# Optimization experiments

Hardware: AMD Instinct MI355X
Metric: run time of the kernel (lower is better)

The kernel has to match this reference:

```python
import jax, jax.numpy as jnp
import numpy as np

K = 3
KK = K * K
EPS = 1e-5


def conv2d(x, w, b, pad):
    y = jax.lax.conv_general_dilated(x, w, (1, 1), [(pad, pad), (pad, pad)],
                                     dimension_numbers=("NCHW", "OIHW", "NCHW"))
    return y + b[None, :, None, None]


def bn(x, g, b, m, v):
    inv = g / jnp.sqrt(v + EPS)
    return x * inv[None, :, None, None] + (b - m * inv)[None, :, None, None]


def deform_sample(x, dy, dx):
    # x: [B,C,H,W]; dy,dx: [B,KK,H,W] -> sampled [B,C,KK,H,W] (bilinear, zeros outside)
    B, C, H, W = x.shape
    k = jnp.arange(K, dtype=x.dtype) - 1.0  # pad=1, dilation=1, stride=1
    ky = jnp.repeat(k, K)  # [KK] row offsets
    kx = jnp.tile(k, K)    # [KK] col offsets
    hh = jnp.arange(H, dtype=x.dtype)
    ww = jnp.arange(W, dtype=x.dtype)
    py = hh[None, :, None] + ky[:, None, None] + dy  # [B,KK,H,W]
    px = ww[None, None, :] + kx[:, None, None] + dx

    def sample_one(img, py, px):
        y0f = jnp.floor(py); x0f = jnp.floor(px)
        wy = py - y0f; wx = px - x0f
        y0 = y0f.astype(jnp.int32); x0 = x0f.astype(jnp.int32)

        def gather(yi, xi, w):
            valid = (yi >= 0) & (yi < H) & (xi >= 0) & (xi < W)
            yc = jnp.clip(yi, 0, H - 1); xc = jnp.clip(xi, 0, W - 1)
            v = img[:, yc, xc]  # [C,KK,H,W]
            return v * (w * valid)[None]

        return (gather(y0, x0, (1 - wy) * (1 - wx)) +
                gather(y0, x0 + 1, (1 - wy) * wx) +
                gather(y0 + 1, x0, wy * (1 - wx)) +
                gather(y0 + 1, x0 + 1, wy * wx))

    return jax.vmap(sample_one)(x, py, px)


def setup_inputs() -> dict:
    key = jax.random.key(0)
    ks = jax.random.split(key, 16)
    B, C, H, W = 8, 256, 64, 64
    d = {
        "feature": jax.random.normal(ks[0], (B, C, H, W), jnp.float32),
        "p1_w": jax.random.normal(ks[1], (C, C, 1, 1), jnp.float32) * 0.05,
        "p1_b": jax.random.normal(ks[2], (C,), jnp.float32) * 0.05,
        "bn1_g": jax.random.normal(ks[3], (C,), jnp.float32) * 0.1 + 1.0,
        "bn1_b": jax.random.normal(ks[4], (C,), jnp.float32) * 0.05,
        "bn1_m": jax.random.normal(ks[5], (C,), jnp.float32) * 0.05,
        "bn1_v": jax.random.uniform(ks[6], (C,), jnp.float32) + 0.5,
        "off_w": jax.random.normal(ks[7], (3 * KK, 2 * C, K, K), jnp.float32) * 0.01,
        "off_b": jax.random.normal(ks[8], (3 * KK,), jnp.float32) * 0.01,
        "dcn_w": jax.random.normal(ks[9], (C, C, K, K), jnp.float32) * 0.05,
        "dcn_b": jax.random.normal(ks[10], (C,), jnp.float32) * 0.05,
        "bn2_g": jax.random.normal(ks[11], (C,), jnp.float32) * 0.1 + 1.0,
        "bn2_b": jax.random.normal(ks[12], (C,), jnp.float32) * 0.05,
        "bn2_m": jax.random.normal(ks[13], (C,), jnp.float32) * 0.05,
        "bn2_v": jax.random.uniform(ks[14], (C,), jnp.float32) + 0.5,
    }
    return d


def reference(feature, p1_w, p1_b, bn1_g, bn1_b, bn1_m, bn1_v,
              off_w, off_b, dcn_w, dcn_b, bn2_g, bn2_b, bn2_m, bn2_v):
    flipped = feature[..., ::-1]                      # flip last (W) axis
    proj = bn(conv2d(feature, p1_w, p1_b, 0), bn1_g, bn1_b, bn1_m, bn1_v)
    # DCNv2: offsets/mask from concat(flipped, proj)
    concat = jnp.concatenate([flipped, proj], axis=1)
    off = conv2d(concat, off_w, off_b, 1)             # [B,27,H,W]
    dy = off[:, :KK]
    dx = off[:, KK:2 * KK]
    mask = jax.nn.sigmoid(off[:, 2 * KK:])            # [B,KK,H,W]
    sampled = deform_sample(flipped, dy, dx)          # [B,C,KK,H,W]
    O = dcn_w.shape[0]
    y = jnp.einsum("bckhw,ock->bohw", sampled * mask[:, None], dcn_w.reshape(O, -1, KK))
    y = y + dcn_b[None, :, None, None]
    y = bn(y, bn2_g, bn2_b, bn2_m, bn2_v)
    return jax.nn.relu(proj + y)
```

## Files before the change

### kernel.cpp

```cpp
#include <hip/hip_runtime.h>
#include <hip/hip_bf16.h>
#include <math.h>

typedef __attribute__((ext_vector_type(8))) short short8;
typedef __attribute__((ext_vector_type(4))) short short4v;
typedef __attribute__((ext_vector_type(4))) float f32x4;
typedef __attribute__((ext_vector_type(2))) float f32x2;

__device__ __forceinline__ float bs2f(short s){
    union { unsigned u; float f; } x; x.u = ((unsigned)(unsigned short)s) << 16; return x.f;
}
__device__ __forceinline__ short f2bs(float f){
    union { float f; unsigned u; } x; x.f = f;
    unsigned r = x.u + 0x7fff + ((x.u >> 16) & 1);
    return (short)(r >> 16);
}
__device__ __forceinline__ f32x2 up2(unsigned u){
    union { unsigned u; float f; } lo, hi;
    lo.u = u << 16; hi.u = u & 0xffff0000u;
    f32x2 r; r.x = lo.f; r.y = hi.f; return r;
}
__device__ __forceinline__ unsigned pk2rn(float lo, float hi){
    __hip_bfloat162 h = __float22bfloat162_rn(make_float2(lo, hi));
    union { __hip_bfloat162 h; unsigned u; } cv; cv.h = h; return cv.u;
}
__device__ __forceinline__ void gl2lds16(const void* g, void* l){
    __builtin_amdgcn_global_load_lds(
        (const __attribute__((address_space(1))) void*)g,
        (__attribute__((address_space(3))) void*)l, 16, 0, 0);
}
__device__ __forceinline__ void hard_barrier(){
    __builtin_amdgcn_sched_barrier(0);
    __builtin_amdgcn_s_barrier();
    __builtin_amdgcn_sched_barrier(0);
}

#define XPB ((size_t)66*66*512)


__global__ void k_prep(const float* __restrict__ p1_w, const float* __restrict__ p1_b,
                       const float* __restrict__ bn1_g, const float* __restrict__ bn1_b,
                       const float* __restrict__ bn1_m, const float* __restrict__ bn1_v,
                       const float* __restrict__ off_w,
                       const float* __restrict__ dcn_w, const float* __restrict__ dcn_b,
                       const float* __restrict__ bn2_g, const float* __restrict__ bn2_b,
                       const float* __restrict__ bn2_m, const float* __restrict__ bn2_v,
                       short* __restrict__ p1_wb, short* __restrict__ Woffb,
                       short* __restrict__ Wbf,
                       float* __restrict__ bias1f, float* __restrict__ inv2f,
                       float* __restrict__ bias2f, unsigned* __restrict__ XpadU)
{
    int blk = blockIdx.x, t = threadIdx.x;
    if (blk == 0) {
        float inv1 = bn1_g[t] / sqrtf(bn1_v[t] + 1e-5f);
        bias1f[t] = p1_b[t] * inv1 + bn1_b[t] - bn1_m[t] * inv1;
        float inv2 = bn2_g[t] / sqrtf(bn2_v[t] + 1e-5f);
        inv2f[t] = inv2;
        bias2f[t] = dcn_b[t] * inv2 + bn2_b[t] - bn2_m[t] * inv2;
    } else if (blk <= 256) {
        int ci = blk - 1;
        float inv1 = bn1_g[t] / sqrtf(bn1_v[t] + 1e-5f);
        p1_wb[t*256 + ci] = f2bs(p1_w[t*256 + ci] * inv1);
    } else if (blk <= 2560) {
        int ck = blk - 257;
        int c = ck / 9, tap = ck % 9;
        Wbf[t*2304 + tap*256 + c] = f2bs(dcn_w[t*2304 + ck]);
    } else if (blk <= 7168) {
        int e = blk - 2561;
        if (t < 32) {
            int tap = e >> 9, ci = e & 511;
            float v = off_w[((t < 27) ? t : 0)*4608 + ci*9 + tap];
            Woffb[t*4608 + e] = (t < 27) ? f2bs(v) : (short)0;
        }
    } else {
        int hb = blk - 7169;
        int b = hb / 260, i = hb % 260;
        int y, x;
        if (i < 66)       { y = 0;  x = i; }
        else if (i < 132) { y = 65; x = i - 66; }
        else { int j = i - 132; y = 1 + (j >> 1); x = (j & 1) * 65; }
        XpadU[((size_t)(b*66 + y)*66 + x)*256 + t] = 0u;
    }
}

__global__ void k_featT(const float* __restrict__ feature, short* __restrict__ Xpad)
{
    __shared__ float tile[64][65];
    int bb = blockIdx.x;
    int cg = bb & 3, h = (bb >> 2) & 63, b = bb >> 8;
    int c0 = cg * 64;
    int t = threadIdx.x;
    int lw = t & 63, li = t >> 6;
    #pragma unroll
    for (int j = 0; j < 16; ++j) {
        int cl = j*4 + li;
        tile[cl][63 - lw] = feature[((b*256 + c0 + cl)*64 + h)*64 + lw];
    }
    __syncthreads();
    #pragma unroll
    for (int j = 0; j < 16; ++j) {
        int wl = j*4 + li;
        Xpad[((size_t)(b*66 + h+1)*66 + (wl+1))*512 + c0 + lw] = f2bs(tile[lw][wl]);
    }
}

__global__ __launch_bounds__(512, 4) void k_projm(
    short* Xpad, const short* __restrict__ p1_wb, const float* __restrict__ bias1f)
{
    __shared__ short Ash[256*32];
    __shared__ short Bsh[64*32];
    int bid = blockIdx.x;
    int b = bid >> 6, h = bid & 63;
    int t = threadIdx.x;
    int lane = t & 63, w = t >> 6;
    int ln = lane & 15, q = lane >> 4;
    int r16 = lane >> 2;
    int sq  = (lane & 3) ^ ((lane >> 3) & 3);
    int rq  = (q ^ ((ln >> 1) & 3)) * 8;
    size_t rowbase = (size_t)(b*66 + h + 1)*66;

    f32x4 acc[2][4] = {};
    for (int kt = 0; kt < 8; ++kt) {
        int kcol = kt*32 + sq*8;
        #pragma unroll
        for (int i = 0; i < 2; ++i) {
            int row = w*32 + i*16 + r16;
            gl2lds16(p1_wb + (size_t)row*256 + kcol, Ash + (w*32 + i*16)*32);
        }
        if (w < 4) {
            int x = w*16 + r16;
            gl2lds16(Xpad + (rowbase + (64 - x))*512 + kcol, Bsh + (w*16)*32);
        }
        __syncthreads();
        short8 af[2], bfr[4];
        #pragma unroll
        for (int i = 0; i < 2; ++i)
            af[i] = *(const short8*)&Ash[(w*32 + i*16 + ln)*32 + rq];
        #pragma unroll
        for (int j = 0; j < 4; ++j)
            bfr[j] = *(const short8*)&Bsh[(j*16 + ln)*32 + rq];
        #pragma unroll
        for (int i = 0; i < 2; ++i)
            #pragma unroll
            for (int j = 0; j < 4; ++j)
                acc[i][j] = __builtin_amdgcn_mfma_f32_16x16x32_bf16(af[i], bfr[j], acc[i][j], 0, 0, 0);
        __syncthreads();
    }
    #pragma unroll
    for (int i = 0; i < 2; ++i) {
        int ob = w*32 + i*16 + q*4;
        #pragma unroll
        for (int j = 0; j < 4; ++j) {
            int x = j*16 + ln;
            size_t xb = (rowbase + x + 1)*512 + 256 + ob;
            short4v st;
            st.x = f2bs(acc[i][j][0] + bias1f[ob]);
            st.y = f2bs(acc[i][j][1] + bias1f[ob+1]);
            st.z = f2bs(acc[i][j][2] + bias1f[ob+2]);
            st.w = f2bs(acc[i][j][3] + bias1f[ob+3]);
            *(short4v*)&Xpad[xb] = st;
        }
    }
}

__global__ __launch_bounds__(512, 4) void k_offm(
    const short* __restrict__ Xpad, const short* __restrict__ Woffb,
    const float* __restrict__ off_b, float* __restrict__ offv)
{
    __shared__ short Ash[2][4][32*32];
    __shared__ short Bsh[2][4][64*32];
    int bid = blockIdx.x;
    int b = bid >> 6, h = bid & 63;
    int t = threadIdx.x;
    int lane = t & 63, w = t >> 6;
    int ln = lane & 15, q = lane >> 4;
    int wr = w >> 2, wc = w & 3;
    int r16 = lane >> 2;
    int sq  = (lane & 3) ^ ((lane >> 3) & 3);
    int rq  = (q ^ ((ln >> 1) & 3)) * 8;
    const short* xb = Xpad + (size_t)b*XPB;

    auto STAGE = [&](int it, int pb){
        int tap = it >> 2, c0 = (it & 3) << 7;
        int dy = tap/3 - 1, dx = tap%3 - 1;
        #pragma unroll
        for (int s = 0; s < 4; ++s) {
            int cc = c0 + s*32 + sq*8;
            if (w < 4) {
                int row = w*16 + r16;
                const short* gB = xb + ((size_t)(h + 1 + dy)*66 + (row + dx + 1))*512 + cc;
                gl2lds16(gB, &Bsh[pb][s][(w*16)*32]);
            } else if (w < 6) {
                int row = (w-4)*16 + r16;
                const short* gA = Woffb + (size_t)row*4608 + tap*512 + cc;
                gl2lds16(gA, &Ash[pb][s][((w-4)*16)*32]);
            }
        }
    };

    f32x4 acc = {};
    STAGE(0, 0);
    asm volatile("s_waitcnt vmcnt(0)" ::: "memory");
    hard_barrier();
    for (int it = 0; it < 36; ++it) {
        int pb = it & 1;
        if (it < 35) STAGE(it + 1, pb ^ 1);
        __builtin_amdgcn_sched_barrier(0);
        #pragma unroll
        for (int s = 0; s < 4; ++s) {
            short8 af  = *(const short8*)&Ash[pb][s][(wr*16 + ln)*32 + rq];
            short8 bfr = *(const short8*)&Bsh[pb][s][(wc*16 + ln)*32 + rq];
            acc = __builtin_amdgcn_mfma_f32_16x16x32_bf16(af, bfr, acc, 0, 0, 0);
        }
        asm volatile("s_waitcnt vmcnt(0) lgkmcnt(0)" ::: "memory");
        hard_barrier();
    }
    int x = wc*16 + ln;
    #pragma unroll
    for (int r = 0; r < 4; ++r) {
        int oc = wr*16 + q*4 + r;
        if (oc < 27)
            offv[((b*27 + oc)*64 + h)*64 + x] = acc[r] + off_b[oc];
    }
}

__global__ __launch_bounds__(512, 4) void k_gemm(
    const short* __restrict__ Xpad,
    const short* __restrict__ Wbf,
    const float* __restrict__ offv,
    const float* __restrict__ inv2f, const float* __restrict__ bias2f,
    float* __restrict__ out)
{
    __shared__ __align__(16) short Ash[2][256*32];
    __shared__ __align__(16) short Bsh[2][64*32];
    __shared__ unsigned c_pk[576];
    __shared__ float c_w[576*4];
    int bid = blockIdx.x;
    int b = bid & 7, h = bid >> 3;
    int t = threadIdx.x;
    int lane = t & 63, w = t >> 6;
    int ln = lane & 15, q = lane >> 4;
    int r16 = lane >> 2;
    int sq  = (lane & 3) ^ ((lane >> 3) & 3);
    int rq  = (q ^ ((ln >> 1) & 3)) * 8;

    for (int e = t; e < 576; e += 512) {
        int p = e / 9, k = e % 9;
        int base = (b*27)*4096 + h*64 + p;
        float dy = offv[base + k*4096];
        float dx = offv[base + (9+k)*4096];
        float ms = offv[base + (18+k)*4096];
        ms = 1.f / (1.f + expf(-ms));
        float py = (float)h + (float)(k/3 - 1) + dy;
        float px = (float)p + (float)(k%3 - 1) + dx;
        float y0f = floorf(py), x0f = floorf(px);
        float wy = py - y0f, wx = px - x0f;
        int y0 = (int)y0f, x0 = (int)x0f;
        int y1 = y0 + 1, x1 = x0 + 1;
        float vy0 = (y0 >= 0 && y0 < 64) ? 1.f : 0.f;
        float vy1 = (y1 >= 0 && y1 < 64) ? 1.f : 0.f;
        float vx0 = (x0 >= 0 && x0 < 64) ? 1.f : 0.f;
        float vx1 = (x1 >= 0 && x1 < 64) ? 1.f : 0.f;
        int y0c = min(max(y0,0),63), y1c = min(max(y1,0),63);
        int x0c = min(max(x0,0),63), x1c = min(max(x1,0),63);
        unsigned cell = (unsigned)(((y0c+1)*66 + x0c+1)*128);
        unsigned sx = (x1c != x0c) ? 1u : 0u;
        unsigned sy = (y1c != y0c) ? 1u : 0u;
        c_pk[e] = cell | (sx << 20) | (sy << 21);
        c_w[e*4+0] = ms * (1.f-wy)*(1.f-wx) * vy0*vx0;
        c_w[e*4+1] = ms * (1.f-wy)*wx       * vy0*vx1;
        c_w[e*4+2] = ms * wy*(1.f-wx)       * vy1*vx0;
        c_w[e*4+3] = ms * wy*wx             * vy1*vx1;
    }
    __syncthreads();

    const uint2* fT = (const uint2*)Xpad + (size_t)b*(XPB/4);
    int pr = t >> 3;
    int jo = t & 7;
    int pe9 = pr*9;
    short* bdst = &Bsh[jo >> 2][pr*32 + (((jo & 3) ^ ((pr >> 1) & 3)) << 3)];

    f32x4 acc[2][4] = {};
    uint4 U[4], V[4];

    auto GATHER = [&](int win, uint4 (&dst)[4]) {
        unsigned pw = c_pk[pe9 + (win >> 2)];
        int o00 = pw & 0xFFFFF;
        int dxs = (pw >> 13) & 128;
        int dys = ((pw >> 8) & 0x2000) | ((pw >> 13) & 0x100);
        int cin = ((win & 3) << 4) + jo*2;
        const uint2* p0 = fT + (o00 + cin);
        dst[0] = *(const uint4*)(p0);
        dst[1] = *(const uint4*)(p0 + dxs);
        dst[2] = *(const uint4*)(p0 + dys);
        dst[3] = *(const uint4*)(p0 + dys + dxs);
    };

    auto WIN = [&](int kc2, uint4 (&uc)[4], uint4 (&vn)[4]) {
        int tap = kc2 >> 2;
        #pragma unroll
        for (int s = 0; s < 2; ++s) {
            int kcol = (kc2*2 + s)*32 + sq*8;
            #pragma unroll
            for (int i = 0; i < 2; ++i) {
                int row = w*32 + i*16 + r16;
                gl2lds16(Wbf + (size_t)row*2304 + kcol, &Ash[s][(w*32 + i*16)*32]);
            }
        }
        __builtin_amdgcn_sched_barrier(0);
        GATHER(kc2 < 35 ? kc2 + 1 : 35, vn);
        const float4 cw = *(const float4*)&c_w[(pe9 + tap)*4];
        f32x2 Wx; Wx.x = cw.x; Wx.y = cw.x;
        f32x2 Wy; Wy.x = cw.y; Wy.y = cw.y;
        f32x2 Wz; Wz.x = cw.z; Wz.y = cw.z;
        f32x2 Ww; Ww.x = cw.w; Ww.y = cw.w;
        f32x2 G0 = Wx*up2(uc[0].x) + Wy*up2(uc[1].x) + Wz*up2(uc[2].x) + Ww*up2(uc[3].x);
        f32x2 G1 = Wx*up2(uc[0].y) + Wy*up2(uc[1].y) + Wz*up2(uc[2].y) + Ww*up2(uc[3].y);
        f32x2 G2 = Wx*up2(uc[0].z) + Wy*up2(uc[1].z) + Wz*up2(uc[2].z) + Ww*up2(uc[3].z);
        f32x2 G3 = Wx*up2(uc[0].w) + Wy*up2(uc[1].w) + Wz*up2(uc[2].w) + Ww*up2(uc[3].w);
        uint4 pkv;
        pkv.x = pk2rn(G0.x, G0.y);
        pkv.y = pk2rn(G1.x, G1.y);
        pkv.z = pk2rn(G2.x, G2.y);
        pkv.w = pk2rn(G3.x, G3.y);
        *(uint4*)bdst = pkv;
        asm volatile("s_waitcnt vmcnt(4) lgkmcnt(0)" ::: "memory");
        hard_barrier();
        #pragma unroll
        for (int s = 0; s < 2; ++s) {
            short8 af[2], bfr[4];
            #pragma unroll
            for (int i = 0; i < 2; ++i)
                af[i] = *(const short8*)&Ash[s][(w*32 + i*16 + ln)*32 + rq];
            #pragma unroll
            for (int jj = 0; jj < 4; ++jj)
                bfr[jj] = *(const short8*)&Bsh[s][(jj*16 + ln)*32 + rq];
            #pragma unroll
            for (int i = 0; i < 2; ++i)
                #pragma unroll
                for (int jj = 0; jj < 4; ++jj)
                    acc[i][jj] = __builtin_amdgcn_mfma_f32_16x16x32_bf16(af[i], bfr[jj], acc[i][jj], 0, 0, 0);
        }
        hard_barrier();
    };

    GATHER(0, U);
    __builtin_amdgcn_sched_barrier(0);
    for (int kc2 = 0; kc2 < 36; kc2 += 2) {
        WIN(kc2, U, V);
        WIN(kc2 + 1, V, U);
    }

    #pragma unroll
    for (int i = 0; i < 2; ++i) {
        int ob = w*32 + i*16 + q*4;
        #pragma unroll
        for (int jj = 0; jj < 4; ++jj) {
            int p = jj*16 + ln;
            size_t xb = ((size_t)(b*66 + h + 1)*66 + p + 1)*512 + 256 + ob;
            short4v prr = *(const short4v*)&Xpad[xb];
            #pragma unroll
            for (int r = 0; r < 4; ++r) {
                int o = ob + r;
                size_t idx = ((size_t)(b*256 + o))*4096 + h*64 + p;
                float rs = bs2f(((const short*)&prr)[r]);
                float v = rs + acc[i][jj][r]*inv2f[o] + bias2f[o];
                out[idx] = v < 0.f ? 0.f : v;
            }
        }
    }
}

extern "C" void kernel_launch(void* const* d_in, const int* in_sizes, int n_in,
                              void* d_out, int out_size, void* d_ws, size_t ws_size,
                              hipStream_t stream)
{
    const float* feature = (const float*)d_in[0];
    const float* p1_w  = (const float*)d_in[1];
    const float* p1_b  = (const float*)d_in[2];
    const float* bn1_g = (const float*)d_in[3];
    const float* bn1_b = (const float*)d_in[4];
    const float* bn1_m = (const float*)d_in[5];
    const float* bn1_v = (const float*)d_in[6];
    const float* off_w = (const float*)d_in[7];
    const float* off_b = (const float*)d_in[8];
    const float* dcn_w = (const float*)d_in[9];
    const float* dcn_b = (const float*)d_in[10];
    const float* bn2_g = (const float*)d_in[11];
    const float* bn2_b = (const float*)d_in[12];
    const float* bn2_m = (const float*)d_in[13];
    const float* bn2_v = (const float*)d_in[14];

    float* ws = (float*)d_ws;
    short* Xpad   = (short*)ws;
    float* offbuf = ws + 8921088;
    short* p1_wb  = (short*)(ws + 9805824);
    short* Woffb  = (short*)(ws + 9838592);
    short* Wbf    = (short*)(ws + 9912320);
    float* bias1f = ws + 10207232;
    float* inv2f  = ws + 10207488;
    float* bias2f = ws + 10207744;

    k_prep<<<9249, 256, 0, stream>>>(p1_w, p1_b, bn1_g, bn1_b, bn1_m, bn1_v,
                                     off_w, dcn_w, dcn_b, bn2_g, bn2_b, bn2_m, bn2_v,
                                     p1_wb, Woffb, Wbf, bias1f, inv2f, bias2f,
                                     (unsigned*)Xpad);
    k_featT<<<2048, 256, 0, stream>>>(feature, Xpad);
    k_projm<<<512, 512, 0, stream>>>(Xpad, p1_wb, bias1f);
    k_offm<<<512, 512, 0, stream>>>(Xpad, Woffb, off_b, offbuf);
    k_gemm<<<512, 512, 0, stream>>>(Xpad, Wbf, offbuf, inv2f, bias2f, (float*)d_out);
}
```

Measured before the change: 235.5 us.

## Load deform GEMM weights directly to registers and double-buffer sampled tiles

In k_gemm, the weight tile is no longer staged through LDS. Each wave loads its A fragments straight from global memory into registers one step ahead. The blended bilinear samples now go into a double-buffered LDS B tile, with the gather issued two steps ahead, so each window needs only one barrier. The offset-conv kernel drops its double buffering for a simpler single-buffer loop with two __syncthreads per iteration, and k_gemm's occupancy hint drops from 4 to 3 blocks for the extra registers. This trades register pressure and less latency hiding in k_offm for fewer barriers and less LDS traffic in the main GEMM.

```diff
diff --git a/kernel.cpp b/kernel.cpp
--- a/kernel.cpp
+++ b/kernel.cpp
@@ -31,6 +31,12 @@
 }
 __device__ __forceinline__ void hard_barrier(){
     __builtin_amdgcn_sched_barrier(0);
+    __builtin_amdgcn_s_barrier();
+    __builtin_amdgcn_sched_barrier(0);
+}
+__device__ __forceinline__ void lds_barrier(){
+    __builtin_amdgcn_sched_barrier(0);
+    asm volatile("s_waitcnt lgkmcnt(0)" ::: "memory");
     __builtin_amdgcn_s_barrier();
     __builtin_amdgcn_sched_barrier(0);
 }
@@ -167,8 +173,8 @@
     const short* __restrict__ Xpad, const short* __restrict__ Woffb,
     const float* __restrict__ off_b, float* __restrict__ offv)
 {
-    __shared__ short Ash[2][4][32*32];
-    __shared__ short Bsh[2][4][64*32];
+    __shared__ short Ash[4][32*32];
+    __shared__ short Bsh[4][64*32];
     int bid = blockIdx.x;
     int b = bid >> 6, h = bid & 63;
     int t = threadIdx.x;
@@ -180,7 +186,8 @@
     int rq  = (q ^ ((ln >> 1) & 3)) * 8;
     const short* xb = Xpad + (size_t)b*XPB;
 
-    auto STAGE = [&](int it, int pb){
+    f32x4 acc = {};
+    for (int it = 0; it < 36; ++it) {
         int tap = it >> 2, c0 = (it & 3) << 7;
         int dy = tap/3 - 1, dx = tap%3 - 1;
         #pragma unroll
@@ -189,31 +196,21 @@
             if (w < 4) {
                 int row = w*16 + r16;
                 const short* gB = xb + ((size_t)(h + 1 + dy)*66 + (row + dx + 1))*512 + cc;
-                gl2lds16(gB, &Bsh[pb][s][(w*16)*32]);
+                gl2lds16(gB, &Bsh[s][(w*16)*32]);
             } else if (w < 6) {
                 int row = (w-4)*16 + r16;
                 const short* gA = Woffb + (size_t)row*4608 + tap*512 + cc;
-                gl2lds16(gA, &Ash[pb][s][((w-4)*16)*32]);
+                gl2lds16(gA, &Ash[s][((w-4)*16)*32]);
             }
         }
-    };
-
-    f32x4 acc = {};
-    STAGE(0, 0);
-    asm volatile("s_waitcnt vmcnt(0)" ::: "memory");
-    hard_barrier();
-    for (int it = 0; it < 36; ++it) {
-        int pb = it & 1;
-        if (it < 35) STAGE(it + 1, pb ^ 1);
-        __builtin_amdgcn_sched_barrier(0);
+        __syncthreads();
         #pragma unroll
         for (int s = 0; s < 4; ++s) {
-            short8 af  = *(const short8*)&Ash[pb][s][(wr*16 + ln)*32 + rq];
-            short8 bfr = *(const short8*)&Bsh[pb][s][(wc*16 + ln)*32 + rq];
+            short8 af  = *(const short8*)&Ash[s][(wr*16 + ln)*32 + rq];
+            short8 bfr = *(const short8*)&Bsh[s][(wc*16 + ln)*32 + rq];
             acc = __builtin_amdgcn_mfma_f32_16x16x32_bf16(af, bfr, acc, 0, 0, 0);
         }
-        asm volatile("s_waitcnt vmcnt(0) lgkmcnt(0)" ::: "memory");
-        hard_barrier();
+        __syncthreads();
     }
     int x = wc*16 + ln;
     #pragma unroll
@@ -224,15 +221,14 @@
     }
 }
 
-__global__ __launch_bounds__(512, 4) void k_gemm(
+__global__ __launch_bounds__(512, 3) void k_gemm(
     const short* __restrict__ Xpad,
     const short* __restrict__ Wbf,
     const float* __restrict__ offv,
     const float* __restrict__ inv2f, const float* __restrict__ bias2f,
     float* __restrict__ out)
 {
-    __shared__ __align__(16) short Ash[2][256*32];
-    __shared__ __align__(16) short Bsh[2][64*32];
+    __shared__ __align__(16) short Bsh[2][2][64*32];
     __shared__ unsigned c_pk[576];
     __shared__ float c_w[576*4];
     int bid = blockIdx.x;
@@ -240,8 +236,6 @@
     int t = threadIdx.x;
     int lane = t & 63, w = t >> 6;
     int ln = lane & 15, q = lane >> 4;
-    int r16 = lane >> 2;
-    int sq  = (lane & 3) ^ ((lane >> 3) & 3);
     int rq  = (q ^ ((ln >> 1) & 3)) * 8;
 
     for (int e = t; e < 576; e += 512) {
@@ -278,10 +272,13 @@
     int pr = t >> 3;
     int jo = t & 7;
     int pe9 = pr*9;
-    short* bdst = &Bsh[jo >> 2][pr*32 + (((jo & 3) ^ ((pr >> 1) & 3)) << 3)];
+    int boff = pr*32 + (((jo & 3) ^ ((pr >> 1) & 3)) << 3);
+    int bs_half = jo >> 2;
+    const short* arow = Wbf + (size_t)(w*32 + ln)*2304 + q*8;
 
     f32x4 acc[2][4] = {};
     uint4 U[4], V[4];
+    short8 A0[2][2], A1[2][2];
 
     auto GATHER = [&](int win, uint4 (&dst)[4]) {
         unsigned pw = c_pk[pe9 + (win >> 2)];
@@ -295,21 +292,15 @@
         dst[2] = *(const uint4*)(p0 + dys);
         dst[3] = *(const uint4*)(p0 + dys + dxs);
     };
-
-    auto WIN = [&](int kc2, uint4 (&uc)[4], uint4 (&vn)[4]) {
-        int tap = kc2 >> 2;
-        #pragma unroll
-        for (int s = 0; s < 2; ++s) {
-            int kcol = (kc2*2 + s)*32 + sq*8;
+    auto ALOAD = [&](int kc, short8 (&af)[2][2]) {
+        #pragma unroll
+        for (int s = 0; s < 2; ++s)
             #pragma unroll
-            for (int i = 0; i < 2; ++i) {
-                int row = w*32 + i*16 + r16;
-                gl2lds16(Wbf + (size_t)row*2304 + kcol, &Ash[s][(w*32 + i*16)*32]);
-            }
-        }
-        __builtin_amdgcn_sched_barrier(0);
-        GATHER(kc2 < 35 ? kc2 + 1 : 35, vn);
-        const float4 cw = *(const float4*)&c_w[(pe9 + tap)*4];
+            for (int i = 0; i < 2; ++i)
+                af[s][i] = *(const short8*)(arow + (size_t)i*16*2304 + kc*64 + s*32);
+    };
+    auto BLEND = [&](uint4 (&uc)[4], int tapW, int bufW) {
+        const float4 cw = *(const float4*)&c_w[(pe9 + tapW)*4];
         f32x2 Wx; Wx.x = cw.x; Wx.y = cw.x;
         f32x2 Wy; Wy.x = cw.y; Wy.y = cw.y;
         f32x2 Wz; Wz.x = cw.z; Wz.y = cw.z;
@@ -323,32 +314,39 @@
         pkv.y = pk2rn(G1.x, G1.y);
         pkv.z = pk2rn(G2.x, G2.y);
         pkv.w = pk2rn(G3.x, G3.y);
-        *(uint4*)bdst = pkv;
-        asm volatile("s_waitcnt vmcnt(4) lgkmcnt(0)" ::: "memory");
-        hard_barrier();
+        *(uint4*)&Bsh[bufW][bs_half][boff] = pkv;
+    };
+    auto WIN = [&](int kc, int bufR, int bufW,
+                   short8 (&afC)[2][2], short8 (&afN)[2][2],
+                   uint4 (&Uc)[4], uint4 (&Un)[4]) {
+        int kn = kc < 35 ? kc + 1 : 35;
+        ALOAD(kn, afN);
+        GATHER(kc < 34 ? kc + 2 : 35, Un);
+        BLEND(Uc, kn >> 2, bufW);
         #pragma unroll
         for (int s = 0; s < 2; ++s) {
-            short8 af[2], bfr[4];
-            #pragma unroll
-            for (int i = 0; i < 2; ++i)
-                af[i] = *(const short8*)&Ash[s][(w*32 + i*16 + ln)*32 + rq];
+            short8 bfr[4];
             #pragma unroll
             for (int jj = 0; jj < 4; ++jj)
-                bfr[jj] = *(const short8*)&Bsh[s][(jj*16 + ln)*32 + rq];
+                bfr[jj] = *(const short8*)&Bsh[bufR][s][(jj*16 + ln)*32 + rq];
             #pragma unroll
             for (int i = 0; i < 2; ++i)
                 #pragma unroll
                 for (int jj = 0; jj < 4; ++jj)
-                    acc[i][jj] = __builtin_amdgcn_mfma_f32_16x16x32_bf16(af[i], bfr[jj], acc[i][jj], 0, 0, 0);
-        }
-        hard_barrier();
+                    acc[i][jj] = __builtin_amdgcn_mfma_f32_16x16x32_bf16(afC[s][i], bfr[jj], acc[i][jj], 0, 0, 0);
+        }
+        lds_barrier();
     };
 
-    GATHER(0, U);
-    __builtin_amdgcn_sched_barrier(0);
-    for (int kc2 = 0; kc2 < 36; kc2 += 2) {
-        WIN(kc2, U, V);
-        WIN(kc2 + 1, V, U);
+    GATHER(0, V);
+    GATHER(1, U);
+    ALOAD(0, A0);
+    BLEND(V, 0, 0);
+    lds_barrier();
+
+    for (int kk = 0; kk < 18; ++kk) {
+        WIN(kk*2,     0, 1, A0, A1, U, V);
+        WIN(kk*2 + 1, 1, 0, A1, A0, V, U);
     }
 
     #pragma unroll
```

Measured after the change: 257.5 us. +9.4%, slower.

## Split offset-conv reduction across warps with direct global fragment loads

Applied to the files above, without the earlier changes.

Rewrites the offset/mask conv kernel so that each of the 8 waves handles a slice of the K dimension (taps × channel chunks). Each wave loads MFMA fragments straight from global memory instead of staging through double-buffered LDS, then the waves reduce their partial accumulators through shared memory. The block-to-(b,h) mapping is also changed so that consecutive blocks cover different batches of the same row. This removes the per-iteration barriers and LDS staging. The cost is uncoalesced-ish 16-byte global loads, a larger shared reduction buffer that may lower occupancy, and redundant weight loads across blocks.

```diff
diff --git a/kernel.cpp b/kernel.cpp
--- a/kernel.cpp
+++ b/kernel.cpp
@@ -167,60 +167,54 @@
     const short* __restrict__ Xpad, const short* __restrict__ Woffb,
     const float* __restrict__ off_b, float* __restrict__ offv)
 {
-    __shared__ short Ash[2][4][32*32];
-    __shared__ short Bsh[2][4][64*32];
+    __shared__ float red[8][64][36];
     int bid = blockIdx.x;
-    int b = bid >> 6, h = bid & 63;
+    int b = bid & 7, h = bid >> 3;
     int t = threadIdx.x;
-    int lane = t & 63, w = t >> 6;
+    int lane = t & 63, g = t >> 6;
     int ln = lane & 15, q = lane >> 4;
-    int wr = w >> 2, wc = w & 3;
-    int r16 = lane >> 2;
-    int sq  = (lane & 3) ^ ((lane >> 3) & 3);
-    int rq  = (q ^ ((ln >> 1) & 3)) * 8;
     const short* xb = Xpad + (size_t)b*XPB;
 
-    auto STAGE = [&](int it, int pb){
-        int tap = it >> 2, c0 = (it & 3) << 7;
+    f32x4 acc[2][4] = {};
+    #pragma unroll 2
+    for (int s8 = 0; s8 < 18; ++s8) {
+        int s = g*18 + s8;
+        int tap = s >> 4, kc = s & 15;
         int dy = tap/3 - 1, dx = tap%3 - 1;
-        #pragma unroll
-        for (int s = 0; s < 4; ++s) {
-            int cc = c0 + s*32 + sq*8;
-            if (w < 4) {
-                int row = w*16 + r16;
-                const short* gB = xb + ((size_t)(h + 1 + dy)*66 + (row + dx + 1))*512 + cc;
-                gl2lds16(gB, &Bsh[pb][s][(w*16)*32]);
-            } else if (w < 6) {
-                int row = (w-4)*16 + r16;
-                const short* gA = Woffb + (size_t)row*4608 + tap*512 + cc;
-                gl2lds16(gA, &Ash[pb][s][((w-4)*16)*32]);
-            }
-        }
-    };
-
-    f32x4 acc = {};
-    STAGE(0, 0);
-    asm volatile("s_waitcnt vmcnt(0)" ::: "memory");
-    hard_barrier();
-    for (int it = 0; it < 36; ++it) {
-        int pb = it & 1;
-        if (it < 35) STAGE(it + 1, pb ^ 1);
-        __builtin_amdgcn_sched_barrier(0);
-        #pragma unroll
-        for (int s = 0; s < 4; ++s) {
-            short8 af  = *(const short8*)&Ash[pb][s][(wr*16 + ln)*32 + rq];
-            short8 bfr = *(const short8*)&Bsh[pb][s][(wc*16 + ln)*32 + rq];
-            acc = __builtin_amdgcn_mfma_f32_16x16x32_bf16(af, bfr, acc, 0, 0, 0);
-        }
-        asm volatile("s_waitcnt vmcnt(0) lgkmcnt(0)" ::: "memory");
-        hard_barrier();
-    }
-    int x = wc*16 + ln;
+        int co = kc*32 + q*8;
+        short8 af[2], bfr[4];
+        #pragma unroll
+        for (int i = 0; i < 2; ++i)
+            af[i] = *(const short8*)(Woffb + (size_t)(i*16 + ln)*4608 + tap*512 + co);
+        #pragma unroll
+        for (int j = 0; j < 4; ++j) {
+            int x = j*16 + ln;
+            bfr[j] = *(const short8*)(xb + ((size_t)(h + 1 + dy)*66 + (x + 1 + dx))*512 + co);
+        }
+        #pragma unroll
+        for (int i = 0; i < 2; ++i)
+            #pragma unroll
+            for (int j = 0; j < 4; ++j)
+                acc[i][j] = __builtin_amdgcn_mfma_f32_16x16x32_bf16(af[i], bfr[j], acc[i][j], 0, 0, 0);
+    }
+
+    #pragma unroll
+    for (int i = 0; i < 2; ++i)
+        #pragma unroll
+        for (int j = 0; j < 4; ++j)
+            *(f32x4*)&red[g][j*16 + ln][i*16 + q*4] = acc[i][j];
+    __syncthreads();
+
+    int x = t & 63, o4 = (t >> 6) * 4;
+    f32x4 sum = *(const f32x4*)&red[0][x][o4];
+    #pragma unroll
+    for (int gg = 1; gg < 8; ++gg)
+        sum += *(const f32x4*)&red[gg][x][o4];
     #pragma unroll
     for (int r = 0; r < 4; ++r) {
-        int oc = wr*16 + q*4 + r;
+        int oc = o4 + r;
         if (oc < 27)
-            offv[((b*27 + oc)*64 + h)*64 + x] = acc[r] + off_b[oc];
+            offv[((b*27 + oc)*64 + h)*64 + x] = sum[r] + off_b[oc];
     }
 }
 
```

Measured after the change: 250.1 us. 6.2% more time.
